# Kernel optimization log

Measured on AMD Instinct MI355X. Metric: run time of the kernel, lower is better.

Reference implementation:

```python
import jax, jax.numpy as jnp
import numpy as np

N_NODES = 100000
N_EDGES = 1000000
DIM = 64


def rel_graph_conv(x, src, dst, etype, W, Ws, b, act):
    # DGL RelGraphConv (regularizer=None, self_loop=True, bias=True, sum agg):
    # out_i = act( sum_{(j->i)} W_{r} x_j + x_i @ Ws + b )
    # num_rels=2: transform once per relation, then select per edge.
    h = jnp.einsum('nd,rdo->rno', x, W)              # [2, N, out]
    m = jnp.where((etype == 0)[:, None], h[0][src], h[1][src])  # [E, out]
    agg = jax.ops.segment_sum(m, dst, num_segments=x.shape[0])  # [N, out]
    out = agg + x @ Ws + b
    return act(out) if act is not None else out


def setup_inputs() -> dict:
    key = jax.random.key(0)
    ks = jax.random.split(key, 16)
    scale = 1.0 / np.sqrt(DIM)
    inp = {
        'features': jax.random.normal(ks[0], (N_NODES, DIM), dtype=jnp.float32),
        'src': jax.random.randint(ks[1], (N_EDGES,), 0, N_NODES, dtype=jnp.int32),
        'dst': jax.random.randint(ks[2], (N_EDGES,), 0, N_NODES, dtype=jnp.int32),
        'etype': jax.random.randint(ks[3], (N_EDGES,), 0, 2, dtype=jnp.int32),
    }
    for i in range(3):
        inp[f'W{i}'] = jax.random.normal(ks[4 + 3 * i], (2, DIM, DIM), dtype=jnp.float32) * scale
        inp[f'Ws{i}'] = jax.random.normal(ks[5 + 3 * i], (DIM, DIM), dtype=jnp.float32) * scale
        inp[f'b{i}'] = jnp.zeros((DIM,), dtype=jnp.float32)
    return inp


def reference(features, src, dst, etype, W0, Ws0, b0, W1, Ws1, b1, W2, Ws2, b2):
    # dropout is identity in eval mode
    h = rel_graph_conv(features, src, dst, etype, W0, Ws0, b0, jax.nn.relu)
    h = rel_graph_conv(h, src, dst, etype, W1, Ws1, b1, jax.nn.relu)
    h = rel_graph_conv(h, src, dst, etype, W2, Ws2, b2, None)
    return h
```

## Files before the change

### kernel.cpp

```cpp
#include <hip/hip_runtime.h>

#define NN 100000
#define NE 1000000
#define DIM 64
#define ZPITCH 200
#define PAD4(c) (((c) + 3) & ~3)
#define CAP 32
#define SENT (2 * NN * CAP)
#define FGRID ((NE / 4 + 255) / 256)
#define G_ZC 196
#define G_CONV 6250

typedef __attribute__((ext_vector_type(4))) float f32x4;
typedef __attribute__((ext_vector_type(8))) _Float16 h8;

union HU4 { uint4 u; h8 h; };

__device__ __forceinline__ ushort f2h(float f) {
    union { _Float16 h; ushort u; } c; c.h = (_Float16)f; return c.u;
}

__global__ __launch_bounds__(256) void front_end(
    int* __restrict__ esrc, int* __restrict__ cnt2,
    const float* __restrict__ x, ushort* __restrict__ xb, ushort* __restrict__ xb1,
    const float* __restrict__ W0, const float* __restrict__ Ws0,
    const float* __restrict__ W1, const float* __restrict__ Ws1,
    const float* __restrict__ W2, const float* __restrict__ Ws2,
    ushort* __restrict__ wt)
{
    int b = blockIdx.x;
    if (b < G_ZC) {
        int i = b * 256 + threadIdx.x;
        if (i < 2 * NN / 4) {
            int4 z = {0, 0, 0, 0};
            *(int4*)(cnt2 + (size_t)i * 4) = z;
        }
    } else if (b < G_ZC + G_CONV) {
        int i = (b - G_ZC) * 256 + threadIdx.x;
        float4 v = ((const float4*)x)[i];
        union { ushort u[4]; uint2 w; } o;
        o.u[0] = f2h(v.x); o.u[1] = f2h(v.y); o.u[2] = f2h(v.z); o.u[3] = f2h(v.w);
        *(uint2*)(xb + (size_t)i * 4) = o.w;
    } else if (b == G_ZC + G_CONV) {
        int t = threadIdx.x;
        if (t < 64) {
            xb[(size_t)NN * DIM + t] = 0;
            xb1[(size_t)NN * DIM + t] = 0;
        } else if (t < 68) {
            esrc[SENT + (t - 64)] = NN;
        }
    } else {
        int idx = (b - G_ZC - G_CONV - 1) * 256 + threadIdx.x;
        int l = idx / 12288, rr = idx % 12288;
        const float* W  = (l == 0) ? W0 : (l == 1) ? W1 : W2;
        const float* Ws = (l == 0) ? Ws0 : (l == 1) ? Ws1 : Ws2;
        int k = rr >> 6, n = rr & 63;
        float v = (k < 128) ? W[k * 64 + n] : Ws[(k - 128) * 64 + n];
        wt[l * 12288 + n * 192 + k] = f2h(v);
    }
}

__global__ __launch_bounds__(256) void fill_direct(const int* __restrict__ src,
                                                   const int* __restrict__ dst,
                                                   const int* __restrict__ et,
                                                   int* __restrict__ cur,
                                                   int* __restrict__ esrc) {
    int e = (blockIdx.x * 256 + threadIdx.x) * 4;
    if (e >= NE) return;
    int4 d4 = *(const int4*)(dst + e);
    int4 t4 = *(const int4*)(et + e);
    int4 s4 = *(const int4*)(src + e);
    int k0 = d4.x * 2 + t4.x;
    int k1 = d4.y * 2 + t4.y;
    int k2 = d4.z * 2 + t4.z;
    int k3 = d4.w * 2 + t4.w;
    int r0 = atomicAdd(&cur[k0], 1);
    int r1 = atomicAdd(&cur[k1], 1);
    int r2 = atomicAdd(&cur[k2], 1);
    int r3 = atomicAdd(&cur[k3], 1);
    esrc[k0 * CAP + r0] = s4.x;
    esrc[k1 * CAP + r1] = s4.y;
    esrc[k2 * CAP + r2] = s4.z;
    esrc[k3 * CAP + r3] = s4.w;
}

__global__ __launch_bounds__(256) void rgcn_aggregate_g4(
    const uint4* __restrict__ xb4, const int* __restrict__ cnt2,
    const int* __restrict__ esrc,
    uint4* __restrict__ agg4)
{
    int t = threadIdx.x, lane = t & 63, wid = t >> 6;
    int g = lane >> 3, s = lane & 7;
    int n = blockIdx.x * 32 + wid * 8 + g;
    int2 c = *(const int2*)(cnt2 + 2 * n);
    int c0 = c.x, c1 = c.y;
    int c0p = PAD4(c0), c1p = PAD4(c1);
    int tmax = c0p > c1p ? c0p : c1p;
    int base0 = n * 2 * CAP;
    int base1 = base0 + CAP;

    const uint4* xrow = xb4 + s;
    HU4 z; z.u.x = 0u; z.u.y = 0u; z.u.z = 0u; z.u.w = 0u;
    h8 a0 = z.h, a1 = z.h;

#pragma unroll 2
    for (int j = 0; j < tmax; j += 4) {
        int i0 = (j < c0p) ? base0 + j : SENT;
        int i1 = (j < c1p) ? base1 + j : SENT;
        int4 qa = *(const int4*)(esrc + i0);
        int4 qb = *(const int4*)(esrc + i1);
        int p0 = (j + 0 < c0) ? qa.x : NN;
        int p1 = (j + 1 < c0) ? qa.y : NN;
        int p2 = (j + 2 < c0) ? qa.z : NN;
        int p3 = (j + 3 < c0) ? qa.w : NN;
        int p4 = (j + 0 < c1) ? qb.x : NN;
        int p5 = (j + 1 < c1) ? qb.y : NN;
        int p6 = (j + 2 < c1) ? qb.z : NN;
        int p7 = (j + 3 < c1) ? qb.w : NN;
        HU4 w0, w1, w2, w3, w4, w5, w6, w7;
        w0.u = xrow[(size_t)p0 * 8];
        w1.u = xrow[(size_t)p1 * 8];
        w2.u = xrow[(size_t)p2 * 8];
        w3.u = xrow[(size_t)p3 * 8];
        w4.u = xrow[(size_t)p4 * 8];
        w5.u = xrow[(size_t)p5 * 8];
        w6.u = xrow[(size_t)p6 * 8];
        w7.u = xrow[(size_t)p7 * 8];
        a0 += w0.h; a0 += w1.h; a0 += w2.h; a0 += w3.h;
        a1 += w4.h; a1 += w5.h; a1 += w6.h; a1 += w7.h;
    }

    HU4 o0, o1; o0.h = a0; o1.h = a1;
    agg4[(size_t)n * 16 + s] = o0.u;
    agg4[(size_t)n * 16 + 8 + s] = o1.u;
}

__global__ __launch_bounds__(256) void rgcn_transform_mfma(
    const ushort* __restrict__ agg,
    const ushort* __restrict__ xb,
    const ushort* __restrict__ wt,
    const float* __restrict__ bias,
    float* __restrict__ outf,
    ushort* __restrict__ xbn,
    int mode)
{
    __shared__ ushort sZ[64 * ZPITCH];

    int t = threadIdx.x, lane = t & 63, wid = t >> 6;
    int quad = lane >> 4, l16 = lane & 15;

    h8 bh[6];
    {
        const ushort* wh = wt + (size_t)(wid * 16 + l16) * 192;
#pragma unroll
        for (int kk = 0; kk < 6; ++kk)
            bh[kk] = *(const h8*)(wh + kk * 32 + quad * 8);
    }
    float bv = bias[wid * 16 + l16];

    int n0 = blockIdx.x * 64;
    for (int i = t; i < 1024; i += 256) {
        int node = i >> 4, c8 = i & 15;
        int n = n0 + node;
        uint4 v = {0u, 0u, 0u, 0u};
        if (n < NN) v = *(const uint4*)(agg + (size_t)n * 128 + c8 * 8);
        *(uint4*)(sZ + node * ZPITCH + c8 * 8) = v;
    }
    for (int i = t; i < 512; i += 256) {
        int node = i >> 3, c8 = i & 7;
        int n = n0 + node;
        uint4 v = {0u, 0u, 0u, 0u};
        if (n < NN) v = *(const uint4*)(xb + (size_t)n * DIM + c8 * 8);
        *(uint4*)(sZ + node * ZPITCH + 128 + c8 * 8) = v;
    }
    __syncthreads();

    f32x4 acc[4];
#pragma unroll
    for (int mt = 0; mt < 4; ++mt) acc[mt] = (f32x4){bv, bv, bv, bv};

#pragma unroll
    for (int kk = 0; kk < 6; ++kk) {
#pragma unroll
        for (int mt = 0; mt < 4; ++mt) {
            h8 a = *(const h8*)(sZ + (mt * 16 + l16) * ZPITCH + kk * 32 + quad * 8);
            acc[mt] = __builtin_amdgcn_mfma_f32_16x16x32_f16(a, bh[kk], acc[mt], 0, 0, 0);
        }
    }

    int col = wid * 16 + l16;
#pragma unroll
    for (int mt = 0; mt < 4; ++mt) {
#pragma unroll
        for (int r = 0; r < 4; ++r) {
            int node = n0 + mt * 16 + quad * 4 + r;
            if (node < NN) {
                float v = acc[mt][r];
                if (mode) outf[(size_t)node * DIM + col] = v;
                else      xbn[(size_t)node * DIM + col] = f2h(fmaxf(v, 0.f));
            }
        }
    }
}

extern "C" void kernel_launch(void* const* d_in, const int* in_sizes, int n_in,
                              void* d_out, int out_size, void* d_ws, size_t ws_size,
                              hipStream_t stream)
{
    const float* feat = (const float*)d_in[0];
    const int*   src  = (const int*)d_in[1];
    const int*   dst  = (const int*)d_in[2];
    const int*   et   = (const int*)d_in[3];
    const float* W[3]  = { (const float*)d_in[4], (const float*)d_in[7], (const float*)d_in[10] };
    const float* Ws[3] = { (const float*)d_in[5], (const float*)d_in[8], (const float*)d_in[11] };
    const float* b[3]  = { (const float*)d_in[6], (const float*)d_in[9], (const float*)d_in[12] };

    uint*   agg   = (uint*)d_ws;
    ushort* xbuf0 = (ushort*)(agg + (size_t)NN * 64);
    ushort* xbuf1 = xbuf0 + (size_t)(NN + 1) * DIM;
    ushort* wt    = xbuf1 + (size_t)(NN + 1) * DIM;
    int* esrc    = (int*)(wt + 3 * 12288);
    int* cnt2    = esrc + 2 * NN * CAP + 4;
    float* outF  = (float*)d_out;

    const dim3 tb(256);
    const int fgrid = G_ZC + G_CONV + 1 + 144;
    const int tgrid = (NN + 63) / 64;
    const int agrid = NN / 32;

    front_end<<<fgrid, tb, 0, stream>>>(esrc, cnt2, feat, xbuf0, xbuf1,
                                        W[0], Ws[0], W[1], Ws[1], W[2], Ws[2], wt);
    fill_direct<<<FGRID, tb, 0, stream>>>(src, dst, et, cnt2, esrc);

    rgcn_aggregate_g4<<<agrid, tb, 0, stream>>>((const uint4*)xbuf0, cnt2, esrc, (uint4*)agg);
    rgcn_transform_mfma<<<tgrid, tb, 0, stream>>>((const ushort*)agg, xbuf0, wt, b[0], nullptr, xbuf1, 0);
    rgcn_aggregate_g4<<<agrid, tb, 0, stream>>>((const uint4*)xbuf1, cnt2, esrc, (uint4*)agg);
    rgcn_transform_mfma<<<tgrid, tb, 0, stream>>>((const ushort*)agg, xbuf1, wt + 12288, b[1], nullptr, xbuf0, 0);
    rgcn_aggregate_g4<<<agrid, tb, 0, stream>>>((const uint4*)xbuf0, cnt2, esrc, (uint4*)agg);
    rgcn_transform_mfma<<<tgrid, tb, 0, stream>>>((const ushort*)agg, xbuf0, wt + 2 * 12288, b[2], outF, nullptr, 1);
}
```

Measured before the change: 284.4 us.

## Transform node features per relation before gathering, fusing self-loop and activation into aggregation

Swaps the layer order from aggregate-then-transform to transform-then-aggregate. A new GEMM kernel computes fp16 per-relation projections h0 and h1 plus the self-loop term (with bias) for every node. The edge list now encodes the relation in the source index, so the aggregate kernel gathers directly from the stacked h0/h1 table, adds the self-loop term, and applies ReLU or writes the fp32 output. This removes the wide 128-column agg intermediate and its reload into the K=192 GEMM. In exchange the gather table doubles in size, and the edge sums are accumulated in fp16 after projection, which may change accuracy.

```diff
diff --git a/kernel.cpp b/kernel.cpp
--- a/kernel.cpp
+++ b/kernel.cpp
@@ -3,12 +3,11 @@
 #define NN 100000
 #define NE 1000000
 #define DIM 64
-#define ZPITCH 200
+#define XPITCH 72
 #define PAD4(c) (((c) + 3) & ~3)
 #define CAP 32
 #define SENT (2 * NN * CAP)
 #define FGRID ((NE / 4 + 255) / 256)
-#define G_ZC 196
 #define G_CONV 6250
 
 typedef __attribute__((ext_vector_type(4))) float f32x4;
@@ -20,43 +19,11 @@
     union { _Float16 h; ushort u; } c; c.h = (_Float16)f; return c.u;
 }
 
-__global__ __launch_bounds__(256) void front_end(
-    int* __restrict__ esrc, int* __restrict__ cnt2,
-    const float* __restrict__ x, ushort* __restrict__ xb, ushort* __restrict__ xb1,
-    const float* __restrict__ W0, const float* __restrict__ Ws0,
-    const float* __restrict__ W1, const float* __restrict__ Ws1,
-    const float* __restrict__ W2, const float* __restrict__ Ws2,
-    ushort* __restrict__ wt)
-{
-    int b = blockIdx.x;
-    if (b < G_ZC) {
-        int i = b * 256 + threadIdx.x;
-        if (i < 2 * NN / 4) {
-            int4 z = {0, 0, 0, 0};
-            *(int4*)(cnt2 + (size_t)i * 4) = z;
-        }
-    } else if (b < G_ZC + G_CONV) {
-        int i = (b - G_ZC) * 256 + threadIdx.x;
-        float4 v = ((const float4*)x)[i];
-        union { ushort u[4]; uint2 w; } o;
-        o.u[0] = f2h(v.x); o.u[1] = f2h(v.y); o.u[2] = f2h(v.z); o.u[3] = f2h(v.w);
-        *(uint2*)(xb + (size_t)i * 4) = o.w;
-    } else if (b == G_ZC + G_CONV) {
-        int t = threadIdx.x;
-        if (t < 64) {
-            xb[(size_t)NN * DIM + t] = 0;
-            xb1[(size_t)NN * DIM + t] = 0;
-        } else if (t < 68) {
-            esrc[SENT + (t - 64)] = NN;
-        }
-    } else {
-        int idx = (b - G_ZC - G_CONV - 1) * 256 + threadIdx.x;
-        int l = idx / 12288, rr = idx % 12288;
-        const float* W  = (l == 0) ? W0 : (l == 1) ? W1 : W2;
-        const float* Ws = (l == 0) ? Ws0 : (l == 1) ? Ws1 : Ws2;
-        int k = rr >> 6, n = rr & 63;
-        float v = (k < 128) ? W[k * 64 + n] : Ws[(k - 128) * 64 + n];
-        wt[l * 12288 + n * 192 + k] = f2h(v);
+__global__ __launch_bounds__(256) void zero_cnt(int* __restrict__ cnt2) {
+    int i = blockIdx.x * 256 + threadIdx.x;
+    if (i < 2 * NN / 4) {
+        int4 z = {0, 0, 0, 0};
+        *(int4*)(cnt2 + (size_t)i * 4) = z;
     }
 }
 
@@ -78,16 +45,120 @@
     int r1 = atomicAdd(&cur[k1], 1);
     int r2 = atomicAdd(&cur[k2], 1);
     int r3 = atomicAdd(&cur[k3], 1);
-    esrc[k0 * CAP + r0] = s4.x;
-    esrc[k1 * CAP + r1] = s4.y;
-    esrc[k2 * CAP + r2] = s4.z;
-    esrc[k3 * CAP + r3] = s4.w;
-}
-
-__global__ __launch_bounds__(256) void rgcn_aggregate_g4(
-    const uint4* __restrict__ xb4, const int* __restrict__ cnt2,
-    const int* __restrict__ esrc,
-    uint4* __restrict__ agg4)
+    esrc[k0 * CAP + r0] = s4.x + t4.x * (NN + 1);
+    esrc[k1 * CAP + r1] = s4.y + t4.y * (NN + 1);
+    esrc[k2 * CAP + r2] = s4.z + t4.z * (NN + 1);
+    esrc[k3 * CAP + r3] = s4.w + t4.w * (NN + 1);
+}
+
+__global__ __launch_bounds__(256) void front_end(
+    int* __restrict__ esrc,
+    const float* __restrict__ x, ushort* __restrict__ xb, ushort* __restrict__ xb1,
+    const float* __restrict__ W0, const float* __restrict__ Ws0,
+    const float* __restrict__ W1, const float* __restrict__ Ws1,
+    const float* __restrict__ W2, const float* __restrict__ Ws2,
+    ushort* __restrict__ wt)
+{
+    int b = blockIdx.x;
+    if (b < G_CONV) {
+        int i = b * 256 + threadIdx.x;
+        float4 v = ((const float4*)x)[i];
+        union { ushort u[4]; uint2 w; } o;
+        o.u[0] = f2h(v.x); o.u[1] = f2h(v.y); o.u[2] = f2h(v.z); o.u[3] = f2h(v.w);
+        *(uint2*)(xb + (size_t)i * 4) = o.w;
+    } else if (b == G_CONV) {
+        int t = threadIdx.x;
+        if (t < 64) {
+            xb[(size_t)NN * DIM + t] = 0;
+            xb1[(size_t)NN * DIM + t] = 0;
+        } else if (t < 68) {
+            esrc[SENT + (t - 64)] = NN;
+        }
+    } else {
+        int idx = (b - G_CONV - 1) * 256 + threadIdx.x;
+        int l = idx / 12288, rr = idx % 12288;
+        const float* W  = (l == 0) ? W0 : (l == 1) ? W1 : W2;
+        const float* Ws = (l == 0) ? Ws0 : (l == 1) ? Ws1 : Ws2;
+        int k = rr >> 6, n = rr & 63;
+        float v = (k < 128) ? W[k * 64 + n] : Ws[(k - 128) * 64 + n];
+        wt[l * 12288 + n * 192 + k] = f2h(v);
+    }
+}
+
+__global__ __launch_bounds__(256) void rgcn_gemm(
+    const ushort* __restrict__ xb,
+    const ushort* __restrict__ wt,
+    const float* __restrict__ bias,
+    ushort* __restrict__ h01,
+    ushort* __restrict__ hs)
+{
+    __shared__ ushort sX[64 * XPITCH];
+
+    int t = threadIdx.x, lane = t & 63, wid = t >> 6;
+    int quad = lane >> 4, l16 = lane & 15;
+
+    h8 b0[2], b1[2], bs[2];
+    {
+        const ushort* wh = wt + (size_t)(wid * 16 + l16) * 192;
+#pragma unroll
+        for (int kk = 0; kk < 2; ++kk) {
+            b0[kk] = *(const h8*)(wh + kk * 32 + quad * 8);
+            b1[kk] = *(const h8*)(wh + 64 + kk * 32 + quad * 8);
+            bs[kk] = *(const h8*)(wh + 128 + kk * 32 + quad * 8);
+        }
+    }
+    float bv = bias[wid * 16 + l16];
+
+    int n0 = blockIdx.x * 64;
+    for (int i = t; i < 512; i += 256) {
+        int node = i >> 3, c8 = i & 7;
+        int n = n0 + node;
+        uint4 v = {0u, 0u, 0u, 0u};
+        if (n <= NN) v = *(const uint4*)(xb + (size_t)n * DIM + c8 * 8);
+        *(uint4*)(sX + node * XPITCH + c8 * 8) = v;
+    }
+    __syncthreads();
+
+    f32x4 a0[4], a1[4], as[4];
+#pragma unroll
+    for (int mt = 0; mt < 4; ++mt) {
+        a0[mt] = (f32x4){0.f, 0.f, 0.f, 0.f};
+        a1[mt] = (f32x4){0.f, 0.f, 0.f, 0.f};
+        as[mt] = (f32x4){bv, bv, bv, bv};
+    }
+
+#pragma unroll
+    for (int mt = 0; mt < 4; ++mt) {
+        h8 x0 = *(const h8*)(sX + (mt * 16 + l16) * XPITCH + quad * 8);
+        h8 x1 = *(const h8*)(sX + (mt * 16 + l16) * XPITCH + 32 + quad * 8);
+        a0[mt] = __builtin_amdgcn_mfma_f32_16x16x32_f16(x0, b0[0], a0[mt], 0, 0, 0);
+        a0[mt] = __builtin_amdgcn_mfma_f32_16x16x32_f16(x1, b0[1], a0[mt], 0, 0, 0);
+        a1[mt] = __builtin_amdgcn_mfma_f32_16x16x32_f16(x0, b1[0], a1[mt], 0, 0, 0);
+        a1[mt] = __builtin_amdgcn_mfma_f32_16x16x32_f16(x1, b1[1], a1[mt], 0, 0, 0);
+        as[mt] = __builtin_amdgcn_mfma_f32_16x16x32_f16(x0, bs[0], as[mt], 0, 0, 0);
+        as[mt] = __builtin_amdgcn_mfma_f32_16x16x32_f16(x1, bs[1], as[mt], 0, 0, 0);
+    }
+
+    int col = wid * 16 + l16;
+#pragma unroll
+    for (int mt = 0; mt < 4; ++mt) {
+#pragma unroll
+        for (int r = 0; r < 4; ++r) {
+            int node = n0 + mt * 16 + quad * 4 + r;
+            if (node <= NN) {
+                h01[(size_t)node * DIM + col] = f2h(a0[mt][r]);
+                h01[(size_t)(NN + 1 + node) * DIM + col] = f2h(a1[mt][r]);
+                if (node < NN) hs[(size_t)node * DIM + col] = f2h(as[mt][r]);
+            }
+        }
+    }
+}
+
+__global__ __launch_bounds__(256) void rgcn_aggregate_f(
+    const uint4* __restrict__ h01_4,
+    const uint4* __restrict__ hs4,
+    const int* __restrict__ cnt2, const int* __restrict__ esrc,
+    ushort* __restrict__ xbn, float* __restrict__ outf, int mode)
 {
     int t = threadIdx.x, lane = t & 63, wid = t >> 6;
     int g = lane >> 3, s = lane & 7;
@@ -99,7 +170,7 @@
     int base0 = n * 2 * CAP;
     int base1 = base0 + CAP;
 
-    const uint4* xrow = xb4 + s;
+    const uint4* xrow = h01_4 + s;
     HU4 z; z.u.x = 0u; z.u.y = 0u; z.u.z = 0u; z.u.w = 0u;
     h8 a0 = z.h, a1 = z.h;
 
@@ -130,76 +201,22 @@
         a1 += w4.h; a1 += w5.h; a1 += w6.h; a1 += w7.h;
     }
 
-    HU4 o0, o1; o0.h = a0; o1.h = a1;
-    agg4[(size_t)n * 16 + s] = o0.u;
-    agg4[(size_t)n * 16 + 8 + s] = o1.u;
-}
-
-__global__ __launch_bounds__(256) void rgcn_transform_mfma(
-    const ushort* __restrict__ agg,
-    const ushort* __restrict__ xb,
-    const ushort* __restrict__ wt,
-    const float* __restrict__ bias,
-    float* __restrict__ outf,
-    ushort* __restrict__ xbn,
-    int mode)
-{
-    __shared__ ushort sZ[64 * ZPITCH];
-
-    int t = threadIdx.x, lane = t & 63, wid = t >> 6;
-    int quad = lane >> 4, l16 = lane & 15;
-
-    h8 bh[6];
-    {
-        const ushort* wh = wt + (size_t)(wid * 16 + l16) * 192;
-#pragma unroll
-        for (int kk = 0; kk < 6; ++kk)
-            bh[kk] = *(const h8*)(wh + kk * 32 + quad * 8);
-    }
-    float bv = bias[wid * 16 + l16];
-
-    int n0 = blockIdx.x * 64;
-    for (int i = t; i < 1024; i += 256) {
-        int node = i >> 4, c8 = i & 15;
-        int n = n0 + node;
-        uint4 v = {0u, 0u, 0u, 0u};
-        if (n < NN) v = *(const uint4*)(agg + (size_t)n * 128 + c8 * 8);
-        *(uint4*)(sZ + node * ZPITCH + c8 * 8) = v;
-    }
-    for (int i = t; i < 512; i += 256) {
-        int node = i >> 3, c8 = i & 7;
-        int n = n0 + node;
-        uint4 v = {0u, 0u, 0u, 0u};
-        if (n < NN) v = *(const uint4*)(xb + (size_t)n * DIM + c8 * 8);
-        *(uint4*)(sZ + node * ZPITCH + 128 + c8 * 8) = v;
-    }
-    __syncthreads();
-
-    f32x4 acc[4];
-#pragma unroll
-    for (int mt = 0; mt < 4; ++mt) acc[mt] = (f32x4){bv, bv, bv, bv};
-
-#pragma unroll
-    for (int kk = 0; kk < 6; ++kk) {
-#pragma unroll
-        for (int mt = 0; mt < 4; ++mt) {
-            h8 a = *(const h8*)(sZ + (mt * 16 + l16) * ZPITCH + kk * 32 + quad * 8);
-            acc[mt] = __builtin_amdgcn_mfma_f32_16x16x32_f16(a, bh[kk], acc[mt], 0, 0, 0);
-        }
-    }
-
-    int col = wid * 16 + l16;
-#pragma unroll
-    for (int mt = 0; mt < 4; ++mt) {
-#pragma unroll
-        for (int r = 0; r < 4; ++r) {
-            int node = n0 + mt * 16 + quad * 4 + r;
-            if (node < NN) {
-                float v = acc[mt][r];
-                if (mode) outf[(size_t)node * DIM + col] = v;
-                else      xbn[(size_t)node * DIM + col] = f2h(fmaxf(v, 0.f));
-            }
-        }
+    HU4 hv; hv.u = hs4[(size_t)n * 8 + s];
+    h8 sum = a0 + a1 + hv.h;
+
+    if (mode == 0) {
+        HU4 o;
+#pragma unroll
+        for (int k = 0; k < 8; ++k) {
+            _Float16 v = sum[k];
+            o.h[k] = v > (_Float16)0 ? v : (_Float16)0;
+        }
+        ((uint4*)xbn)[(size_t)n * 8 + s] = o.u;
+    } else {
+        float4 f0 = {(float)sum[0], (float)sum[1], (float)sum[2], (float)sum[3]};
+        float4 f1 = {(float)sum[4], (float)sum[5], (float)sum[6], (float)sum[7]};
+        *(float4*)(outf + (size_t)n * DIM + s * 8) = f0;
+        *(float4*)(outf + (size_t)n * DIM + s * 8 + 4) = f1;
     }
 }
 
@@ -215,8 +232,9 @@
     const float* Ws[3] = { (const float*)d_in[5], (const float*)d_in[8], (const float*)d_in[11] };
     const float* b[3]  = { (const float*)d_in[6], (const float*)d_in[9], (const float*)d_in[12] };
 
-    uint*   agg   = (uint*)d_ws;
-    ushort* xbuf0 = (ushort*)(agg + (size_t)NN * 64);
+    ushort* h01   = (ushort*)d_ws;
+    ushort* hs    = h01 + (size_t)(2 * NN + 2) * DIM;
+    ushort* xbuf0 = hs + (size_t)NN * DIM;
     ushort* xbuf1 = xbuf0 + (size_t)(NN + 1) * DIM;
     ushort* wt    = xbuf1 + (size_t)(NN + 1) * DIM;
     int* esrc    = (int*)(wt + 3 * 12288);
@@ -224,18 +242,22 @@
     float* outF  = (float*)d_out;
 
     const dim3 tb(256);
-    const int fgrid = G_ZC + G_CONV + 1 + 144;
-    const int tgrid = (NN + 63) / 64;
+    const int fgrid = G_CONV + 1 + 144;
+    const int ggrid = (NN + 63) / 64;
     const int agrid = NN / 32;
 
-    front_end<<<fgrid, tb, 0, stream>>>(esrc, cnt2, feat, xbuf0, xbuf1,
+    zero_cnt<<<196, tb, 0, stream>>>(cnt2);
+    fill_direct<<<FGRID, tb, 0, stream>>>(src, dst, et, cnt2, esrc);
+    front_end<<<fgrid, tb, 0, stream>>>(esrc, feat, xbuf0, xbuf1,
                                         W[0], Ws[0], W[1], Ws[1], W[2], Ws[2], wt);
-    fill_direct<<<FGRID, tb, 0, stream>>>(src, dst, et, cnt2, esrc);
-
-    rgcn_aggregate_g4<<<agrid, tb, 0, stream>>>((const uint4*)xbuf0, cnt2, esrc, (uint4*)agg);
-    rgcn_transform_mfma<<<tgrid, tb, 0, stream>>>((const ushort*)agg, xbuf0, wt, b[0], nullptr, xbuf1, 0);
-    rgcn_aggregate_g4<<<agrid, tb, 0, stream>>>((const uint4*)xbuf1, cnt2, esrc, (uint4*)agg);
-    rgcn_transform_mfma<<<tgrid, tb, 0, stream>>>((const ushort*)agg, xbuf1, wt + 12288, b[1], nullptr, xbuf0, 0);
-    rgcn_aggregate_g4<<<agrid, tb, 0, stream>>>((const uint4*)xbuf0, cnt2, esrc, (uint4*)agg);
-    rgcn_transform_mfma<<<tgrid, tb, 0, stream>>>((const ushort*)agg, xbuf0, wt + 2 * 12288, b[2], outF, nullptr, 1);
-}
+
+    rgcn_gemm<<<ggrid, tb, 0, stream>>>(xbuf0, wt, b[0], h01, hs);
+    rgcn_aggregate_f<<<agrid, tb, 0, stream>>>((const uint4*)h01, (const uint4*)hs,
+                                               cnt2, esrc, xbuf1, nullptr, 0);
+    rgcn_gemm<<<ggrid, tb, 0, stream>>>(xbuf1, wt + 12288, b[1], h01, hs);
+    rgcn_aggregate_f<<<agrid, tb, 0, stream>>>((const uint4*)h01, (const uint4*)hs,
+                                               cnt2, esrc, xbuf0, nullptr, 0);
+    rgcn_gemm<<<ggrid, tb, 0, stream>>>(xbuf0, wt + 2 * 12288, b[2], h01, hs);
+    rgcn_aggregate_f<<<agrid, tb, 0, stream>>>((const uint4*)h01, (const uint4*)hs,
+                                               cnt2, esrc, nullptr, outF, 1);
+}
```

Result: slower. 304.1 us (+6.9%).
